# Optimization experiments

Hardware: AMD Instinct MI355X
Metric: run time of the kernel (lower is better)

Reference implementation:

```python
import jax, jax.numpy as jnp
import numpy as np

TOPK = 8

def setup_inputs() -> dict:
    key = jax.random.key(0)
    k1, k2, k3, k4, k5 = jax.random.split(key, 5)
    B, S, D, E = 8, 2048, 4096, 64
    scale = 1.0 / np.sqrt(D)
    x = jax.random.normal(k1, (B, S, D), dtype=jnp.float32)
    Wr = jax.random.uniform(k2, (D, E), dtype=jnp.float32, minval=-scale, maxval=scale)
    br = jax.random.uniform(k3, (E,), dtype=jnp.float32, minval=-scale, maxval=scale)
    Wn = jax.random.uniform(k4, (D, E), dtype=jnp.float32, minval=-scale, maxval=scale)
    bn = jax.random.uniform(k5, (E,), dtype=jnp.float32, minval=-scale, maxval=scale)
    return {"x": x, "Wr": Wr, "br": br, "Wn": Wn, "bn": bn}

def reference(x, Wr, br, Wn, bn):
    B, S, D = x.shape
    E = Wr.shape[1]
    logits = jnp.einsum('bsd,de->bse', x, Wr) + br          # [B,S,E]
    # NOTE: original module computes noisy_logits = logits + randn*noisy_vec but
    # then takes topk/softmax on the CLEAN logits, so the noise branch is dead code.
    noisy_vec = jnp.einsum('bsd,de->bse', x, Wn) + bn       # computed, unused (faithful)
    del noisy_vec
    topk_vals, topk_idx = jax.lax.top_k(logits, TOPK)       # [B,S,K]
    T = B * S
    flat_vals = topk_vals.reshape(T, TOPK)
    flat_idx = topk_idx.reshape(T, TOPK)
    sparse = jnp.full((T, E), -jnp.inf, dtype=logits.dtype)
    sparse = sparse.at[jnp.arange(T)[:, None], flat_idx].set(flat_vals)
    router_scores = jax.nn.softmax(sparse, axis=-1).reshape(B, S, E)
    return router_scores, topk_idx
```

## Files before the change

### kernel.cpp

```cpp
#include <hip/hip_runtime.h>
#include <math.h>

#define DDIM 4096
#define EDIM 64
#define NROWS 16384
#define NS 4
#define KC (DDIM / NS)
#define DT 128
#define TOPK_K 8

__global__ __launch_bounds__(256) void router_pass1(
    const float* __restrict__ x, const float* __restrict__ Wr,
    float* __restrict__ partial) {
  const int tid  = threadIdx.x;
  const int lane = tid & 63;
  const int wave = tid >> 6;
  const int row0 = blockIdx.x * 64;
  const int k0   = blockIdx.y * KC;
  const int e0 = __builtin_amdgcn_readfirstlane(wave * 16);

  __shared__ float4 xs[64 * (DT / 4)];

  float acc[16];
  #pragma unroll
  for (int e = 0; e < 16; ++e) acc[e] = 0.f;

  for (int t = 0; t < KC; t += DT) {
    __syncthreads();
    #pragma unroll
    for (int i = 0; i < (64 * (DT / 4)) / 256; ++i) {
      int fi = tid + i * 256;
      int r  = fi >> 5;
      int c  = fi & 31;
      float4 v = *(const float4*)(x + (size_t)(row0 + r) * DDIM + k0 + t + c * 4);
      xs[r * 32 + (c ^ (r & 7))] = v;
    }
    __syncthreads();
    for (int c = 0; c < DT / 4; ++c) {
      float4 xv = xs[lane * 32 + (c ^ (lane & 7))];
      int dg = k0 + t + c * 4;
      #pragma unroll
      for (int j = 0; j < 4; ++j) {
        const float* wrow = Wr + (size_t)(dg + j) * EDIM + e0;
        float xj = (j == 0) ? xv.x : (j == 1) ? xv.y : (j == 2) ? xv.z : xv.w;
        #pragma unroll
        for (int e = 0; e < 16; ++e)
          acc[e] = fmaf(xj, wrow[e], acc[e]);
      }
    }
  }
  float* p = partial + ((size_t)blockIdx.y * NROWS + row0 + lane) * EDIM + e0;
  #pragma unroll
  for (int e = 0; e < 16; e += 4)
    *(float4*)(p + e) = make_float4(acc[e], acc[e + 1], acc[e + 2], acc[e + 3]);
}

__global__ __launch_bounds__(256) void router_pass2(
    const float* __restrict__ partial, const float* __restrict__ br,
    float* __restrict__ out_scores, float* __restrict__ out_idx) {
  const int lane = threadIdx.x & 63;
  const int row  = blockIdx.x * 4 + (threadIdx.x >> 6);

  float v = br[lane];
  #pragma unroll
  for (int s = 0; s < NS; ++s)
    v += partial[((size_t)s * NROWS + row) * EDIM + lane];

  const float v0 = v;
  float cur = v;
  bool sel  = false;
  int myidx = 0;
  float maxv = 0.f;

  #pragma unroll
  for (int k = 0; k < TOPK_K; ++k) {
    float bv = cur;
    int   bi = lane;
    #pragma unroll
    for (int off = 32; off; off >>= 1) {
      float ov = __shfl_xor(bv, off);
      int   oi = __shfl_xor(bi, off);
      if (ov > bv || (ov == bv && oi < bi)) { bv = ov; bi = oi; }
    }
    if (k == 0) maxv = bv;
    if (lane == k) myidx = bi;
    if (lane == bi) { cur = -__builtin_inff(); sel = true; }
  }

  float p = sel ? expf(v0 - maxv) : 0.f;
  float ssum = p;
  #pragma unroll
  for (int off = 32; off; off >>= 1) ssum += __shfl_xor(ssum, off);

  out_scores[(size_t)row * EDIM + lane] = p / ssum;
  if (lane < TOPK_K)
    out_idx[(size_t)row * TOPK_K + lane] = (float)myidx;
}

extern "C" void kernel_launch(void* const* d_in, const int* in_sizes, int n_in,
                              void* d_out, int out_size, void* d_ws, size_t ws_size,
                              hipStream_t stream) {
  const float* x  = (const float*)d_in[0];
  const float* Wr = (const float*)d_in[1];
  const float* br = (const float*)d_in[2];

  float* partial    = (float*)d_ws;
  float* out_scores = (float*)d_out;
  float* out_idx    = out_scores + (size_t)NROWS * EDIM;

  dim3 g1(NROWS / 64, NS);
  router_pass1<<<g1, 256, 0, stream>>>(x, Wr, partial);
  router_pass2<<<NROWS / 4, 256, 0, stream>>>(partial, br, out_scores, out_idx);
}
```

Baseline: 144.3 us.

## Emulate fp32 router GEMM with multi-digit int8 MFMA and fuse top-k softmax

Replaces the scalar-FMA split-K GEMM and separate top-k kernel with one fused kernel. It converts x and Wr to fixed-point values split into byte digits and accumulates the cross-digit products with int8 MFMA instructions. Wr is pre-packed into an MFMA-friendly layout by a small conversion kernel, then staged into LDS with double-buffered global_load_lds. The logits are recombined in double precision and top-k and softmax run in the same kernel, which removes the partial-sum round trip and the second launch. The risk is accuracy: the fixed-point scaling truncates or saturates values and dropped low-order digit products can differ from fp32 results, which could flip top-k choices.

```diff
diff --git a/kernel.cpp b/kernel.cpp
--- a/kernel.cpp
+++ b/kernel.cpp
@@ -4,97 +4,184 @@
 #define DDIM 4096
 #define EDIM 64
 #define NROWS 16384
-#define NS 4
-#define KC (DDIM / NS)
-#define DT 128
+#define MBLK 32
+#define NKT 32
 #define TOPK_K 8
-
-__global__ __launch_bounds__(256) void router_pass1(
-    const float* __restrict__ x, const float* __restrict__ Wr,
-    float* __restrict__ partial) {
+#define DIGIT_BIAS 0x00808080
+
+typedef int i32x4 __attribute__((ext_vector_type(4)));
+
+__device__ __forceinline__ int digits_of(float f) {
+  int v = __float2int_rn(f);
+  return (v + DIGIT_BIAS) ^ DIGIT_BIAS;
+}
+
+__device__ __forceinline__ unsigned perm_b32(unsigned a, unsigned b, unsigned sel) {
+#if __has_builtin(__builtin_amdgcn_perm)
+  return __builtin_amdgcn_perm(a, b, sel);
+#else
+  union { unsigned u[2]; unsigned char c[8]; } s; s.u[0] = b; s.u[1] = a;
+  unsigned r = 0;
+  for (int i = 0; i < 4; ++i) r |= (unsigned)s.c[(sel >> (8*i)) & 7] << (8*i);
+  return r;
+#endif
+}
+
+__global__ __launch_bounds__(256) void wr_convert(const float* __restrict__ Wr,
+                                                  char* __restrict__ wl8) {
+  int t = blockIdx.x * 256 + threadIdx.x;
+  int e = t & 63, k16 = t >> 6;
+  int kt64 = k16 >> 2, kgg = k16 & 3, nf = e >> 4, col = e & 15;
+  int D[16];
+  #pragma unroll
+  for (int j = 0; j < 16; ++j)
+    D[j] = digits_of(Wr[(size_t)(k16 * 16 + j) * EDIM + e] * 68719476736.0f);
+  #pragma unroll
+  for (int pl = 0; pl < 4; ++pl) {
+    unsigned wv[4];
+    #pragma unroll
+    for (int g = 0; g < 4; ++g)
+      wv[g] = ((unsigned)((D[4*g+0] >> (8*pl)) & 255))
+            | ((unsigned)((D[4*g+1] >> (8*pl)) & 255) << 8)
+            | ((unsigned)((D[4*g+2] >> (8*pl)) & 255) << 16)
+            | ((unsigned)((D[4*g+3] >> (8*pl)) & 255) << 24);
+    i32x4 val = {(int)wv[0], (int)wv[1], (int)wv[2], (int)wv[3]};
+    *(i32x4*)(wl8 + (size_t)pl * 262144 + (size_t)(kt64 * 4 + nf) * 1024
+              + (size_t)(kgg * 16 + col) * 16) = val;
+  }
+}
+
+__global__ __launch_bounds__(512, 4) void router_fused(
+    const float* __restrict__ x, const char* __restrict__ wl8,
+    const float* __restrict__ br,
+    float* __restrict__ out_scores, float* __restrict__ out_idx) {
+  __shared__ __align__(16) char smem[2][32768];
+
   const int tid  = threadIdx.x;
   const int lane = tid & 63;
-  const int wave = tid >> 6;
-  const int row0 = blockIdx.x * 64;
-  const int k0   = blockIdx.y * KC;
-  const int e0 = __builtin_amdgcn_readfirstlane(wave * 16);
-
-  __shared__ float4 xs[64 * (DT / 4)];
-
-  float acc[16];
-  #pragma unroll
-  for (int e = 0; e < 16; ++e) acc[e] = 0.f;
-
-  for (int t = 0; t < KC; t += DT) {
-    __syncthreads();
-    #pragma unroll
-    for (int i = 0; i < (64 * (DT / 4)) / 256; ++i) {
-      int fi = tid + i * 256;
-      int r  = fi >> 5;
-      int c  = fi & 31;
-      float4 v = *(const float4*)(x + (size_t)(row0 + r) * DDIM + k0 + t + c * 4);
-      xs[r * 32 + (c ^ (r & 7))] = v;
+  const int w    = tid >> 6;
+  const int mw   = w >> 2;
+  const int nw   = w & 3;
+  const int kg   = lane >> 4;
+  const size_t row_g = (size_t)blockIdx.x * MBLK + mw * 16 + (lane & 15);
+  const float* xbase = x + row_g * DDIM + kg * 16;
+  const float bias = br[nw * 16 + (lane & 15)];
+
+  i32x4 s6{}, s5{}, s4{}, s3{}, s2{};
+
+  auto stage = [&](int t, int b) {
+    #pragma unroll
+    for (int i = 0; i < 4; ++i) {
+      int c = w * 4 + i;
+      int plane = c >> 3, half = (c >> 2) & 1, nf = c & 3;
+      const char* src = wl8 + (size_t)plane * 262144 +
+                        (size_t)((2 * t + half) * 4 + nf) * 1024 + (size_t)lane * 16;
+      __builtin_amdgcn_global_load_lds(
+          (const __attribute__((address_space(1))) unsigned int*)(const void*)src,
+          (__attribute__((address_space(3))) unsigned int*)(void*)&smem[b][c * 1024],
+          16, 0, 0);
+    }
+  };
+
+  stage(0, 0);
+  __syncthreads();
+
+  for (int t = 0; t < NKT; ++t) {
+    const int cb = t & 1;
+    if (t + 1 < NKT) stage(t + 1, cb ^ 1);
+
+    float4 xf[8];
+    const float* p = xbase + t * 128;
+    #pragma unroll
+    for (int h = 0; h < 2; ++h)
+      #pragma unroll
+      for (int g = 0; g < 4; ++g)
+        xf[h * 4 + g] = *(const float4*)(p + h * 64 + g * 4);
+
+    const char* base = smem[cb];
+    #pragma unroll
+    for (int h = 0; h < 2; ++h) {
+      i32x4 a0, a1, a2, a3;
+      #pragma unroll
+      for (int g = 0; g < 4; ++g) {
+        float4 v = xf[h * 4 + g];
+        unsigned f0 = (unsigned)digits_of(v.x * 33554432.0f);
+        unsigned f1 = (unsigned)digits_of(v.y * 33554432.0f);
+        unsigned f2 = (unsigned)digits_of(v.z * 33554432.0f);
+        unsigned f3 = (unsigned)digits_of(v.w * 33554432.0f);
+        unsigned zl01 = perm_b32(f1, f0, 0x05010400u);
+        unsigned zh01 = perm_b32(f1, f0, 0x07030602u);
+        unsigned zl23 = perm_b32(f3, f2, 0x05010400u);
+        unsigned zh23 = perm_b32(f3, f2, 0x07030602u);
+        a0[g] = (int)perm_b32(zl23, zl01, 0x05040100u);
+        a1[g] = (int)perm_b32(zl23, zl01, 0x07060302u);
+        a2[g] = (int)perm_b32(zh23, zh01, 0x05040100u);
+        a3[g] = (int)perm_b32(zh23, zh01, 0x07060302u);
+      }
+      i32x4 b0 = *(const i32x4*)(base + (0 * 8 + h * 4 + nw) * 1024 + lane * 16);
+      i32x4 b1 = *(const i32x4*)(base + (1 * 8 + h * 4 + nw) * 1024 + lane * 16);
+      i32x4 b2 = *(const i32x4*)(base + (2 * 8 + h * 4 + nw) * 1024 + lane * 16);
+      i32x4 b3 = *(const i32x4*)(base + (3 * 8 + h * 4 + nw) * 1024 + lane * 16);
+
+      s6 = __builtin_amdgcn_mfma_i32_16x16x64_i8(a3, b3, s6, 0, 0, 0);
+      s5 = __builtin_amdgcn_mfma_i32_16x16x64_i8(a3, b2, s5, 0, 0, 0);
+      s5 = __builtin_amdgcn_mfma_i32_16x16x64_i8(a2, b3, s5, 0, 0, 0);
+      s4 = __builtin_amdgcn_mfma_i32_16x16x64_i8(a3, b1, s4, 0, 0, 0);
+      s4 = __builtin_amdgcn_mfma_i32_16x16x64_i8(a2, b2, s4, 0, 0, 0);
+      s4 = __builtin_amdgcn_mfma_i32_16x16x64_i8(a1, b3, s4, 0, 0, 0);
+      s3 = __builtin_amdgcn_mfma_i32_16x16x64_i8(a3, b0, s3, 0, 0, 0);
+      s3 = __builtin_amdgcn_mfma_i32_16x16x64_i8(a2, b1, s3, 0, 0, 0);
+      s3 = __builtin_amdgcn_mfma_i32_16x16x64_i8(a1, b2, s3, 0, 0, 0);
+      s3 = __builtin_amdgcn_mfma_i32_16x16x64_i8(a0, b3, s3, 0, 0, 0);
+      s2 = __builtin_amdgcn_mfma_i32_16x16x64_i8(a2, b0, s2, 0, 0, 0);
+      s2 = __builtin_amdgcn_mfma_i32_16x16x64_i8(a1, b1, s2, 0, 0, 0);
+      s2 = __builtin_amdgcn_mfma_i32_16x16x64_i8(a0, b2, s2, 0, 0, 0);
     }
     __syncthreads();
-    for (int c = 0; c < DT / 4; ++c) {
-      float4 xv = xs[lane * 32 + (c ^ (lane & 7))];
-      int dg = k0 + t + c * 4;
+  }
+
+  double* ls = (double*)smem;
+  #pragma unroll
+  for (int j = 0; j < 4; ++j) {
+    int r = mw * 16 + (lane >> 4) * 4 + j;
+    int c = nw * 16 + (lane & 15);
+    double lg = (double)s6[j] * 0x1p-13 + (double)s5[j] * 0x1p-21
+              + (double)s4[j] * 0x1p-29 + (double)s3[j] * 0x1p-37
+              + (double)s2[j] * 0x1p-45 + (double)bias;
+    ls[r * 64 + c] = lg;
+  }
+  __syncthreads();
+
+  for (int rr = 0; rr < 4; ++rr) {
+    int r = w * 4 + rr;
+    double v0 = ls[r * 64 + lane];
+    double cur = v0;
+    bool sel  = false;
+    int myidx = 0;
+    double maxv = 0.0;
+    #pragma unroll
+    for (int k = 0; k < TOPK_K; ++k) {
+      double bv = cur;
+      int    bi = lane;
       #pragma unroll
-      for (int j = 0; j < 4; ++j) {
-        const float* wrow = Wr + (size_t)(dg + j) * EDIM + e0;
-        float xj = (j == 0) ? xv.x : (j == 1) ? xv.y : (j == 2) ? xv.z : xv.w;
-        #pragma unroll
-        for (int e = 0; e < 16; ++e)
-          acc[e] = fmaf(xj, wrow[e], acc[e]);
+      for (int off = 32; off; off >>= 1) {
+        double ov = __shfl_xor(bv, off);
+        int    oi = __shfl_xor(bi, off);
+        if (ov > bv || (ov == bv && oi < bi)) { bv = ov; bi = oi; }
       }
+      if (k == 0) maxv = bv;
+      if (lane == k) myidx = bi;
+      if (lane == bi) { cur = -__builtin_inf(); sel = true; }
     }
-  }
-  float* p = partial + ((size_t)blockIdx.y * NROWS + row0 + lane) * EDIM + e0;
-  #pragma unroll
-  for (int e = 0; e < 16; e += 4)
-    *(float4*)(p + e) = make_float4(acc[e], acc[e + 1], acc[e + 2], acc[e + 3]);
-}
-
-__global__ __launch_bounds__(256) void router_pass2(
-    const float* __restrict__ partial, const float* __restrict__ br,
-    float* __restrict__ out_scores, float* __restrict__ out_idx) {
-  const int lane = threadIdx.x & 63;
-  const int row  = blockIdx.x * 4 + (threadIdx.x >> 6);
-
-  float v = br[lane];
-  #pragma unroll
-  for (int s = 0; s < NS; ++s)
-    v += partial[((size_t)s * NROWS + row) * EDIM + lane];
-
-  const float v0 = v;
-  float cur = v;
-  bool sel  = false;
-  int myidx = 0;
-  float maxv = 0.f;
-
-  #pragma unroll
-  for (int k = 0; k < TOPK_K; ++k) {
-    float bv = cur;
-    int   bi = lane;
-    #pragma unroll
-    for (int off = 32; off; off >>= 1) {
-      float ov = __shfl_xor(bv, off);
-      int   oi = __shfl_xor(bi, off);
-      if (ov > bv || (ov == bv && oi < bi)) { bv = ov; bi = oi; }
-    }
-    if (k == 0) maxv = bv;
-    if (lane == k) myidx = bi;
-    if (lane == bi) { cur = -__builtin_inff(); sel = true; }
-  }
-
-  float p = sel ? expf(v0 - maxv) : 0.f;
-  float ssum = p;
-  #pragma unroll
-  for (int off = 32; off; off >>= 1) ssum += __shfl_xor(ssum, off);
-
-  out_scores[(size_t)row * EDIM + lane] = p / ssum;
-  if (lane < TOPK_K)
-    out_idx[(size_t)row * TOPK_K + lane] = (float)myidx;
+    float pv = sel ? expf((float)(v0 - maxv)) : 0.f;
+    float ssum = pv;
+    #pragma unroll
+    for (int off = 32; off; off >>= 1) ssum += __shfl_xor(ssum, off);
+
+    size_t rg = (size_t)blockIdx.x * MBLK + r;
+    out_scores[rg * 64 + lane] = pv / ssum;
+    if (lane < TOPK_K) out_idx[rg * 8 + lane] = (float)myidx;
+  }
 }
 
 extern "C" void kernel_launch(void* const* d_in, const int* in_sizes, int n_in,
@@ -104,11 +191,10 @@
   const float* Wr = (const float*)d_in[1];
   const float* br = (const float*)d_in[2];
 
-  float* partial    = (float*)d_ws;
+  char* wl8 = (char*)d_ws;
   float* out_scores = (float*)d_out;
   float* out_idx    = out_scores + (size_t)NROWS * EDIM;
 
-  dim3 g1(NROWS / 64, NS);
-  router_pass1<<<g1, 256, 0, stream>>>(x, Wr, partial);
-  router_pass2<<<NROWS / 4, 256, 0, stream>>>(partial, br, out_scores, out_idx);
-}
+  wr_convert<<<64, 256, 0, stream>>>(Wr, wl8);
+  router_fused<<<NROWS / MBLK, 512, 0, stream>>>(x, wl8, br, out_scores, out_idx);
+}
```

New measurement: 190.5 us. 1.32x slower.
